# Kernel tuning notes

Hardware: AMD Instinct MI355X
Metric: run time of the kernel (lower is better)

The kernel has to match this reference:

```python
import jax, jax.numpy as jnp
import numpy as np

NUM_HEADS = 16


def setup_inputs() -> dict:
    key = jax.random.key(0)
    k1, k2, k3 = jax.random.split(key, 3)
    B, N, D = 4, 2048, 1024
    x = jax.random.normal(k1, (B, N, D), dtype=jnp.float32)
    Wqkv = jax.random.normal(k2, (3 * D, D), dtype=jnp.float32) * 0.02
    bqkv = jax.random.normal(k3, (3 * D,), dtype=jnp.float32) * 0.02
    return {"x": x, "Wqkv": Wqkv, "bqkv": bqkv}


def reference(x, Wqkv, bqkv):
    B, N, D = x.shape
    H = NUM_HEADS
    pd = D // H
    # fused QKV projection: nn.Linear applies x @ W^T + b
    qkv = x @ Wqkv.T + bqkv                      # (B, N, 3D)
    qkv = qkv.reshape(B, N, 3, H, pd).transpose(2, 0, 3, 1, 4)  # (3, B, H, N, pd)
    q, k, v = qkv[0], qkv[1], qkv[2]
    # NOTE: original applies NO 1/sqrt(pd) scaling — preserved faithfully.
    scores = jnp.einsum('bhnd,bhmd->bhnm', q, k)  # (B, H, N, N)
    att = jax.nn.softmax(scores, axis=-1)
    # The original's broadcast-multiply + sum(dim=2) is exactly att @ v.
    out = jnp.einsum('bhnm,bhmd->bhnd', att, v)   # (B, H, N, pd)
    # Faithful to the original buggy reshape: (B,H,N,pd) -> (B,N,D) with NO transpose.
    return out.reshape(B, N, D)
```

## Files before the change

### kernel.cpp

```cpp
#include <hip/hip_runtime.h>

typedef unsigned short u16;
typedef unsigned int u32;
typedef _Float16 f16;
typedef __attribute__((ext_vector_type(8))) f16 half8;
typedef __attribute__((ext_vector_type(4))) f16 half4;
typedef __attribute__((ext_vector_type(4))) float f32x4;

#define MFMA16(a, b, c) __builtin_amdgcn_mfma_f32_16x16x32_f16((a), (b), (c), 0, 0, 0)

static __device__ __forceinline__ void gload16(const void* g, void* l) {
  __builtin_amdgcn_global_load_lds(
      (const __attribute__((address_space(1))) void*)g,
      (__attribute__((address_space(3))) void*)l, 16, 0, 0);
}
static __device__ __forceinline__ half8 lds8h(const f16* base, int row, int colb) {
  int phys = row * 128 + (colb ^ ((row & 7) << 4));
  return *(const half8*)((const char*)base + phys);
}

__global__ void cvt_kernel(const float* __restrict__ in, f16* __restrict__ o, int n4) {
  int i = blockIdx.x * blockDim.x + threadIdx.x;
  int stride = gridDim.x * blockDim.x;
  for (; i < n4; i += stride) {
    float4 v = ((const float4*)in)[i];
    half4 h;
    h.x = (f16)v.x; h.y = (f16)v.y; h.z = (f16)v.z; h.w = (f16)v.w;
    *(half4*)(o + (size_t)i * 4) = h;
  }
}

__global__ __launch_bounds__(256, 2) void gemm_qkv(
    const f16* __restrict__ xf, const f16* __restrict__ wf,
    const float* __restrict__ bias,
    f16* __restrict__ qf, f16* __restrict__ kf, f16* __restrict__ vf) {
  __shared__ __align__(16) f16 sA[128 * 64];
  __shared__ __align__(16) f16 sB[128 * 64];
  const int L = blockIdx.x;
  const int swz = (L & 7) * 192 + (L >> 3);
  const int ct = swz % 24, mt = swz / 24;
  const int c0 = ct * 128, m0 = mt * 128;
  const int tid = threadIdx.x, lane = tid & 63, w = tid >> 6;
  const int wm = w >> 1, wn = w & 1;
  f32x4 acc[4][4] = {};

  for (int t = 0; t < 16; ++t) {
    const int k0 = t * 64;
    for (int j = 0; j < 4; ++j) {
      int chunk = w * 4 + j;
      int r = chunk * 8 + (lane >> 3);
      int cb = (lane & 7) * 16;
      int cbs = cb ^ ((r & 7) << 4);
      gload16((const char*)(xf + (size_t)(m0 + r) * 1024 + k0) + cbs, (char*)sA + chunk * 1024);
      gload16((const char*)(wf + (size_t)(c0 + r) * 1024 + k0) + cbs, (char*)sB + chunk * 1024);
    }
    asm volatile("s_waitcnt vmcnt(0)" ::: "memory");
    __syncthreads();

    for (int ki = 0; ki < 2; ++ki) {
      const int colb = (ki * 32 + (lane >> 4) * 8) * 2;
      half8 a[4], bfr[4];
      for (int mi = 0; mi < 4; ++mi)
        a[mi] = lds8h(sA, wm * 64 + mi * 16 + (lane & 15), colb);
      for (int ni = 0; ni < 4; ++ni)
        bfr[ni] = lds8h(sB, wn * 64 + ni * 16 + (lane & 15), colb);
      for (int mi = 0; mi < 4; ++mi)
        for (int ni = 0; ni < 4; ++ni)
          acc[mi][ni] = MFMA16(a[mi], bfr[ni], acc[mi][ni]);
    }
    __syncthreads();
  }

  const int g = lane >> 4, cl = lane & 15;
  const int b = m0 >> 11;
  const int n0t = (m0 & 2047) >> 6;
  const int t = n0t + wm;
  const bool isV = (ct >= 16);
  if (!isV) {
    for (int ni = 0; ni < 4; ++ni) {
      const int c = c0 + wn * 64 + ni * 16 + cl;
      const float bv = bias[c];
      f16* d = (c < 1024) ? qf : kf;
      const int p = c & 63, h = (c & 1023) >> 6;
      const int kki = p >> 5, lhi = (p >> 3) & 3, e = p & 7;
      for (int mi = 0; mi < 4; ++mi) {
        size_t base = (((size_t)(b * 16 + h) * 32 + t) * 8 + (size_t)kki * 4 + mi) * 512
                      + (size_t)lhi * 128 + e;
        for (int i = 0; i < 4; ++i)
          d[base + (size_t)(g * 4 + i) * 8] = (f16)(acc[mi][ni][i] + bv);
      }
    }
  } else {
    for (int ni = 0; ni < 4; ++ni) {
      const int c = c0 + wn * 64 + ni * 16 + cl;
      const float bv = bias[c];
      const int cv = c - 2048, h = cv >> 6, p = cv & 63;
      const int niv = p >> 4, lane_lo = p & 15;
      for (int mi = 0; mi < 4; ++mi) {
        const int kki = mi >> 1;
        for (int i = 0; i < 4; ++i) {
          const int lhi = (mi & 1) * 2 + (g >> 1);
          const int e = (g & 1) * 4 + i;
          size_t a = (((size_t)(b * 16 + h) * 32 + t) * 8 + (size_t)kki * 4 + niv) * 512
                     + (size_t)(lhi * 16 + lane_lo) * 8 + e;
          vf[a] = (f16)(acc[mi][ni][i] + bv);
        }
      }
    }
  }
}

__global__ __launch_bounds__(256, 4) void attn_kernel(
    const f16* __restrict__ qf, const f16* __restrict__ kf,
    const f16* __restrict__ vf, float* __restrict__ out) {
  __shared__ __align__(16) f16 pbuf[4][32 * 72];

  const int tid = threadIdx.x, lane = tid & 63, w = tid >> 6;
  const int bid = blockIdx.x;
  const int xcd = bid & 7, li = bid >> 3;
  const int bh = xcd * 8 + (li >> 4);
  const int qt = li & 15;
  const int g = lane >> 4, q = lane & 15;
  const size_t bhbase = (size_t)bh * 32 * 4096;

  half8 qfr[2][2];
  for (int mi = 0; mi < 2; ++mi) {
    int idx = 2 * w + mi;
    int t = qt * 2 + (idx >> 2), nni = idx & 3;
    for (int ki = 0; ki < 2; ++ki) {
      size_t a = bhbase + (((size_t)t * 2 + ki) * 4 + nni) * 512 + (size_t)lane * 8;
      qfr[mi][ki] = *(const half8*)(qf + a);
    }
  }

  f32x4 oaccT[2][4] = {};
  float mrow[2], lrow[2];
  for (int mi = 0; mi < 2; ++mi) { mrow[mi] = -3.0e38f; lrow[mi] = 0.f; }

  for (int t = 0; t < 32; ++t) {
    const size_t tb = bhbase + (size_t)t * 4096;

    f32x4 sacc[2][4] = {};
    for (int ki = 0; ki < 2; ++ki) {
      half8 khf[4];
      for (int ni = 0; ni < 4; ++ni)
        khf[ni] = *(const half8*)(kf + tb + (((size_t)ki * 4 + ni) * 64 + lane) * 8);
      for (int mi = 0; mi < 2; ++mi)
        for (int ni = 0; ni < 4; ++ni)
          sacc[mi][ni] = MFMA16(khf[ni], qfr[mi][ki], sacc[mi][ni]);
    }

    half8 vfr[2][4];
    for (int ki = 0; ki < 2; ++ki)
      for (int ni = 0; ni < 4; ++ni)
        vfr[ki][ni] = *(const half8*)(vf + tb + (((size_t)ki * 4 + ni) * 64 + lane) * 8);

    for (int mi = 0; mi < 2; ++mi) {
      float a0 = fmaxf(fmaxf(sacc[mi][0][0], sacc[mi][0][1]), fmaxf(sacc[mi][0][2], sacc[mi][0][3]));
      float a1 = fmaxf(fmaxf(sacc[mi][1][0], sacc[mi][1][1]), fmaxf(sacc[mi][1][2], sacc[mi][1][3]));
      float a2 = fmaxf(fmaxf(sacc[mi][2][0], sacc[mi][2][1]), fmaxf(sacc[mi][2][2], sacc[mi][2][3]));
      float a3 = fmaxf(fmaxf(sacc[mi][3][0], sacc[mi][3][1]), fmaxf(sacc[mi][3][2], sacc[mi][3][3]));
      float mx = fmaxf(fmaxf(a0, a1), fmaxf(a2, a3));
      mx = fmaxf(mx, __shfl_xor(mx, 16));
      mx = fmaxf(mx, __shfl_xor(mx, 32));
      float mnew = fmaxf(mrow[mi], mx);
      float corr = __expf(mrow[mi] - mnew);
      mrow[mi] = mnew;
      float rs = 0.f;
      const int prow = mi * 16 + q;
      for (int ni = 0; ni < 4; ++ni) {
        float p0 = __expf(sacc[mi][ni][0] - mnew);
        float p1 = __expf(sacc[mi][ni][1] - mnew);
        float p2 = __expf(sacc[mi][ni][2] - mnew);
        float p3 = __expf(sacc[mi][ni][3] - mnew);
        rs += (p0 + p1) + (p2 + p3);
        half4 pk;
        pk.x = (f16)p0; pk.y = (f16)p1; pk.z = (f16)p2; pk.w = (f16)p3;
        *(half4*)&pbuf[w][prow * 72 + ni * 16 + g * 4] = pk;
      }
      rs += __shfl_xor(rs, 16);
      rs += __shfl_xor(rs, 32);
      lrow[mi] = lrow[mi] * corr + rs;
      for (int ni = 0; ni < 4; ++ni)
        for (int i = 0; i < 4; ++i) oaccT[mi][ni][i] *= corr;
    }

    for (int ki = 0; ki < 2; ++ki) {
      half8 pf[2];
      for (int mi = 0; mi < 2; ++mi)
        pf[mi] = *(const half8*)&pbuf[w][(mi * 16 + q) * 72 + ki * 32 + g * 8];
      for (int ni = 0; ni < 4; ++ni)
        for (int mi = 0; mi < 2; ++mi)
          oaccT[mi][ni] = MFMA16(vfr[ki][ni], pf[mi], oaccT[mi][ni]);
    }
  }

  for (int mi = 0; mi < 2; ++mi) {
    float inv = 1.f / lrow[mi];
    int grow = qt * 128 + w * 32 + mi * 16 + q;
    size_t obase = ((size_t)bh * 2048 + grow) * 64;
    for (int ni = 0; ni < 4; ++ni)
      for (int i = 0; i < 4; ++i)
        out[obase + ni * 16 + g * 4 + i] = oaccT[mi][ni][i] * inv;
  }
}

extern "C" void kernel_launch(void* const* d_in, const int* in_sizes, int n_in,
                              void* d_out, int out_size, void* d_ws, size_t ws_size,
                              hipStream_t stream) {
  (void)in_sizes; (void)n_in; (void)out_size; (void)ws_size;
  const float* x = (const float*)d_in[0];
  const float* Wqkv = (const float*)d_in[1];
  const float* bqkv = (const float*)d_in[2];
  float* out = (float*)d_out;

  f16* xf = (f16*)d_ws;
  f16* wf = xf + 8388608;
  f16* qf = wf + 3145728;
  f16* kf = qf + 8388608;
  f16* vf = kf + 8388608;

  cvt_kernel<<<2048, 256, 0, stream>>>(x, xf, 8388608 / 4);
  cvt_kernel<<<768, 256, 0, stream>>>(Wqkv, wf, 3145728 / 4);
  gemm_qkv<<<1536, 256, 0, stream>>>(xf, wf, bqkv, qf, kf, vf);
  attn_kernel<<<1024, 256, 0, stream>>>(qf, kf, vf, out);
}
```

Measured before the change: 254.4 us.

## Stage QKV epilogue through LDS for coalesced stores; lazy softmax rescale

The GEMM epilogue now writes the biased fp16 results into shared memory in the attention-friendly tiled layout, then each wave copies contiguous 4 KB tiles to global memory with 16-byte stores. This replaces scattered 2-byte global writes. Separately, the attention kernel skips the running-max update and the rescale of the accumulators and row sums when no new row max exceeds the stored max by more than 8. That saves exp calls and multiplies in most iterations, but lets exponents reach up to e^8 before rescaling, which slightly raises the risk of fp16 overflow in P.

```diff
diff --git a/kernel.cpp b/kernel.cpp
--- a/kernel.cpp
+++ b/kernel.cpp
@@ -34,8 +34,9 @@
     const f16* __restrict__ xf, const f16* __restrict__ wf,
     const float* __restrict__ bias,
     f16* __restrict__ qf, f16* __restrict__ kf, f16* __restrict__ vf) {
-  __shared__ __align__(16) f16 sA[128 * 64];
-  __shared__ __align__(16) f16 sB[128 * 64];
+  __shared__ __align__(16) f16 smem[16384];
+  f16* sA = smem;
+  f16* sB = smem + 8192;
   const int L = blockIdx.x;
   const int swz = (L & 7) * 192 + (L >> 3);
   const int ct = swz % 24, mt = swz / 24;
@@ -74,39 +75,48 @@
   const int g = lane >> 4, cl = lane & 15;
   const int b = m0 >> 11;
   const int n0t = (m0 & 2047) >> 6;
-  const int t = n0t + wm;
-  const bool isV = (ct >= 16);
-  if (!isV) {
+  const int reg = wn * 2 + wm;
+  if (ct < 16) {
     for (int ni = 0; ni < 4; ++ni) {
       const int c = c0 + wn * 64 + ni * 16 + cl;
       const float bv = bias[c];
-      f16* d = (c < 1024) ? qf : kf;
-      const int p = c & 63, h = (c & 1023) >> 6;
+      const int p = ni * 16 + cl;
       const int kki = p >> 5, lhi = (p >> 3) & 3, e = p & 7;
       for (int mi = 0; mi < 4; ++mi) {
-        size_t base = (((size_t)(b * 16 + h) * 32 + t) * 8 + (size_t)kki * 4 + mi) * 512
-                      + (size_t)lhi * 128 + e;
+        int off = reg * 4096 + (kki * 4 + mi) * 512 + lhi * 128 + e;
         for (int i = 0; i < 4; ++i)
-          d[base + (size_t)(g * 4 + i) * 8] = (f16)(acc[mi][ni][i] + bv);
+          smem[off + (g * 4 + i) * 8] = (f16)(acc[mi][ni][i] + bv);
       }
     }
   } else {
     for (int ni = 0; ni < 4; ++ni) {
       const int c = c0 + wn * 64 + ni * 16 + cl;
       const float bv = bias[c];
-      const int cv = c - 2048, h = cv >> 6, p = cv & 63;
+      const int p = ni * 16 + cl;
       const int niv = p >> 4, lane_lo = p & 15;
       for (int mi = 0; mi < 4; ++mi) {
         const int kki = mi >> 1;
         for (int i = 0; i < 4; ++i) {
           const int lhi = (mi & 1) * 2 + (g >> 1);
           const int e = (g & 1) * 4 + i;
-          size_t a = (((size_t)(b * 16 + h) * 32 + t) * 8 + (size_t)kki * 4 + niv) * 512
-                     + (size_t)(lhi * 16 + lane_lo) * 8 + e;
-          vf[a] = (f16)(acc[mi][ni][i] + bv);
+          smem[reg * 4096 + (kki * 4 + niv) * 512 + (lhi * 16 + lane_lo) * 8 + e] =
+              (f16)(acc[mi][ni][i] + bv);
         }
       }
     }
+  }
+  __syncthreads();
+  {
+    const int rw = (w & 1) * 2 + (w >> 1);
+    const int h_idx = rw >> 1, t_idx = rw & 1;
+    f16* dst; int hbase;
+    if (ct < 8)       { dst = qf; hbase = c0 >> 6; }
+    else if (ct < 16) { dst = kf; hbase = (c0 - 1024) >> 6; }
+    else              { dst = vf; hbase = (c0 - 2048) >> 6; }
+    size_t gbase = (((size_t)(b * 16 + hbase + h_idx) * 32) + (size_t)(n0t + t_idx)) * 4096;
+    for (int j = 0; j < 8; ++j)
+      *(float4*)(dst + gbase + (size_t)j * 512 + (size_t)lane * 8) =
+          *(const float4*)(smem + rw * 4096 + j * 512 + lane * 8);
   }
 }
 
@@ -163,9 +173,17 @@
       float mx = fmaxf(fmaxf(a0, a1), fmaxf(a2, a3));
       mx = fmaxf(mx, __shfl_xor(mx, 16));
       mx = fmaxf(mx, __shfl_xor(mx, 32));
-      float mnew = fmaxf(mrow[mi], mx);
-      float corr = __expf(mrow[mi] - mnew);
-      mrow[mi] = mnew;
+      float mnew;
+      if (__all(mx <= mrow[mi] + 8.f)) {
+        mnew = mrow[mi];
+      } else {
+        mnew = fmaxf(mrow[mi], mx);
+        float corr = __expf(mrow[mi] - mnew);
+        mrow[mi] = mnew;
+        lrow[mi] *= corr;
+        for (int ni = 0; ni < 4; ++ni)
+          for (int i = 0; i < 4; ++i) oaccT[mi][ni][i] *= corr;
+      }
       float rs = 0.f;
       const int prow = mi * 16 + q;
       for (int ni = 0; ni < 4; ++ni) {
@@ -180,9 +198,7 @@
       }
       rs += __shfl_xor(rs, 16);
       rs += __shfl_xor(rs, 32);
-      lrow[mi] = lrow[mi] * corr + rs;
-      for (int ni = 0; ni < 4; ++ni)
-        for (int i = 0; i < 4; ++i) oaccT[mi][ni][i] *= corr;
+      lrow[mi] += rs;
     }
 
     for (int ki = 0; ki < 2; ++ki) {
```

Result: slower. 260.2 us (+2.3%).
